# Performance work log

Hardware: AMD Instinct MI355X
Metric: run time of the kernel (lower is better)

The kernel has to match this reference:

```python
import jax, jax.numpy as jnp
import numpy as np

N = 20000
E = 100000
EB = 20000
WIDTH = 32
KER_W = 64
KER_IN = 6
DEPTH = 4


def setup_inputs() -> dict:
    key = jax.random.key(0)
    ks = jax.random.split(key, 24)
    d = {}
    d["x"] = jax.random.normal(ks[0], (N, 1), dtype=jnp.float32)
    d["edge_index"] = jax.random.randint(ks[1], (2, E), 0, N)
    d["edge_attr"] = jax.random.uniform(ks[2], (E, KER_IN), dtype=jnp.float32)
    d["edge_index_boundary"] = jax.random.randint(ks[3], (2, EB), 0, N)
    d["edge_attr_boundary"] = jax.random.uniform(ks[4], (EB, KER_IN), dtype=jnp.float32)
    s = 0.1
    d["fc1_w"] = jax.random.normal(ks[5], (1, WIDTH), dtype=jnp.float32) * s
    d["fc1_b"] = jnp.zeros((WIDTH,), jnp.float32)
    d["fc2_w"] = jax.random.normal(ks[6], (WIDTH, 1), dtype=jnp.float32) * s
    d["fc2_b"] = jnp.zeros((1,), jnp.float32)
    for i, pfx in enumerate(["k1", "k2"]):
        o = 7 + i * 5
        d[pfx + "_w1"] = jax.random.normal(ks[o], (KER_IN, KER_W), dtype=jnp.float32) * s
        d[pfx + "_b1"] = jnp.zeros((KER_W,), jnp.float32)
        d[pfx + "_w2"] = jax.random.normal(ks[o + 1], (KER_W, KER_W), dtype=jnp.float32) * s
        d[pfx + "_b2"] = jnp.zeros((KER_W,), jnp.float32)
        d[pfx + "_w3"] = jax.random.normal(ks[o + 2], (KER_W, WIDTH * WIDTH), dtype=jnp.float32) * s
        d[pfx + "_b3"] = jnp.zeros((WIDTH * WIDTH,), jnp.float32)
        d[("root1", "root2")[i]] = jax.random.normal(ks[o + 3], (WIDTH, WIDTH), dtype=jnp.float32) * s
        d[("bias1", "bias2")[i]] = jnp.zeros((WIDTH,), jnp.float32)
    return d


def _nnconv(h, ei, ea, w1, b1, w2, b2, w3, b3, root, bias):
    # kernel MLP on edge_attr -> per-edge [in, out] weight
    k = jax.nn.relu(ea @ w1 + b1)
    k = jax.nn.relu(k @ w2 + b2)
    w = (k @ w3 + b3).reshape(-1, WIDTH, WIDTH)  # [E, in, out]
    msg = jnp.einsum('ei,eio->eo', h[ei[0]], w)  # gather + per-edge matmul
    agg = jax.ops.segment_sum(msg, ei[1], num_segments=N)
    cnt = jax.ops.segment_sum(jnp.ones((ei.shape[1],), h.dtype), ei[1], num_segments=N)
    agg = agg / jnp.maximum(cnt, 1.0)[:, None]  # mean aggregation
    return agg + h @ root + bias


def reference(x, edge_index, edge_attr, edge_index_boundary, edge_attr_boundary,
              fc1_w, fc1_b, fc2_w, fc2_b,
              k1_w1, k1_b1, k1_w2, k1_b2, k1_w3, k1_b3, root1, bias1,
              k2_w1, k2_b1, k2_w2, k2_b2, k2_w3, k2_b3, root2, bias2):
    h0 = x @ fc1_w + fc1_b  # fc1(data.x), reused every depth step
    h = h0
    for _ in range(DEPTH):
        h = (_nnconv(h, edge_index, edge_attr, k1_w1, k1_b1, k1_w2, k1_b2, k1_w3, k1_b3, root1, bias1)
             + _nnconv(h, edge_index_boundary, edge_attr_boundary, k2_w1, k2_b1, k2_w2, k2_b2, k2_w3, k2_b3, root2, bias2))
        h = jax.nn.relu(h) + h0
    return h @ fc2_w + fc2_b
```

## Files before the change

### kernel.cpp

```cpp
#include <hip/hip_runtime.h>
#include <cstdint>
#include <cstddef>

#define NN    20000
#define EM    100000
#define EBN   20000
#define WID   32
#define KW    64
#define KIN   6
#define NDEPTH 4
#define GC    2080
#define NBL   8
#define GR    2084
#define NQ    520
#define TPB_F 576


__global__ void k_count4(const int* __restrict__ ei, const int* __restrict__ eib,
                         int* __restrict__ cs1, int* __restrict__ cnt1,
                         int* __restrict__ csb, int* __restrict__ cntb) {
    int t = blockIdx.x * blockDim.x + threadIdx.x;
    if (t < EM) atomicAdd(&cs1[ei[t]], 1);
    else if (t < 2 * EM) atomicAdd(&cnt1[ei[t]], 1);
    else if (t < 2 * EM + EBN) atomicAdd(&csb[eib[t - 2 * EM]], 1);
    else if (t < 2 * EM + 2 * EBN) atomicAdd(&cntb[eib[t - 2 * EM]], 1);
}

__global__ void k_inv2(const int* __restrict__ cnt1, float* __restrict__ inv1,
                       const int* __restrict__ cntb, float* __restrict__ invb) {
    int i = blockIdx.x * blockDim.x + threadIdx.x;
    if (i < NN) {
        int c = cnt1[i]; if (c < 1) c = 1;
        inv1[i] = 1.0f / (float)c;
    } else if (i < 2 * NN) {
        int c = cntb[i - NN]; if (c < 1) c = 1;
        invb[i - NN] = 1.0f / (float)c;
    }
}


__global__ __launch_bounds__(1024) void k_scan3(
        const int* __restrict__ csA, int* __restrict__ curA, int* __restrict__ arankA,
        int* __restrict__ anodesA, int* __restrict__ aoffA, int* __restrict__ dnaA, int EA,
        const int* __restrict__ csB, int* __restrict__ curB, int* __restrict__ arankB,
        int* __restrict__ anodesB, int* __restrict__ aoffB, int* __restrict__ dnaB, int EB) {
    __shared__ int part[1024];
    __shared__ int partf[1024];
    const int* cnt; int *cur, *arank, *anodes, *aoff, *dna; int E;
    if (blockIdx.x == 0) { cnt = csA; cur = curA; arank = arankA; anodes = anodesA; aoff = aoffA; dna = dnaA; E = EA; }
    else                 { cnt = csB; cur = curB; arank = arankB; anodes = anodesB; aoff = aoffB; dna = dnaB; E = EB; }
    int t = threadIdx.x;
    int per = (NN + 1023) / 1024;
    int base = t * per;
    int s = 0, f = 0;
    for (int i = 0; i < per; i++) {
        int idx = base + i;
        if (idx < NN) { int c = cnt[idx]; s += c; f += (c > 0) ? 1 : 0; }
    }
    part[t] = s; partf[t] = f;
    __syncthreads();
    for (int od = 1; od < 1024; od <<= 1) {
        int v  = (t >= od) ? part[t - od] : 0;
        int vf = (t >= od) ? partf[t - od] : 0;
        __syncthreads();
        part[t] += v; partf[t] += vf;
        __syncthreads();
    }
    int run  = (t > 0) ? part[t - 1] : 0;
    int runf = (t > 0) ? partf[t - 1] : 0;
    for (int i = 0; i < per; i++) {
        int idx = base + i;
        if (idx < NN) {
            int c = cnt[idx];
            cur[idx] = run;
            arank[idx] = runf;
            if (c > 0) { anodes[runf] = idx; aoff[runf] = run; runf++; }
            run += c;
        }
    }
    if (t == 1023) { dna[0] = partf[1023]; aoff[partf[1023]] = E; }
}


__global__ void k_scatter3(const int* __restrict__ ei, int* __restrict__ cur1,
                           int* __restrict__ perm1, const int* __restrict__ eib,
                           int* __restrict__ curb, int* __restrict__ permb) {
    int t = blockIdx.x * blockDim.x + threadIdx.x;
    if (t < EM) { int p = atomicAdd(&cur1[ei[t]], 1); perm1[p] = t; }
    else if (t < EM + EBN) {
        int e = t - EM;
        int p = atomicAdd(&curb[eib[e]], 1); permb[p] = e;
    }
}

__global__ void k_permidx3(const int* __restrict__ ei, const int* __restrict__ perm1,
                           const int* __restrict__ arank1, int* __restrict__ rk1,
                           int* __restrict__ dst1,
                           const int* __restrict__ eib, const int* __restrict__ permb,
                           const int* __restrict__ arankb, int* __restrict__ rkb,
                           int* __restrict__ dstb) {
    int t = blockIdx.x * blockDim.x + threadIdx.x;
    if (t < EM) {
        int e = perm1[t];
        rk1[t] = arank1[ei[e]];
        dst1[t] = ei[EM + e];
    } else if (t < EM + EBN) {
        int i = t - EM;
        int e = permb[i];
        rkb[i] = arankb[eib[e]];
        dstb[i] = eib[EBN + e];
    }
}


__global__ void k_permM3(const float* __restrict__ w3a, const float* __restrict__ b3a,
                         float* __restrict__ M1,
                         const float* __restrict__ w3b, const float* __restrict__ b3b,
                         float* __restrict__ M2,
                         const float* __restrict__ r1, const float* __restrict__ b1,
                         const float* __restrict__ r2, const float* __restrict__ b2,
                         float* __restrict__ rs, float* __restrict__ bs) {
    int t = blockIdx.x * blockDim.x + threadIdx.x;
    if (t < 32 * GC) {
        int i = t / GC, c = t % GC;
        M1[t] = (c < 2048) ? w3a[(c >> 5) * 1024 + i * 32 + (c & 31)]
                           : b3a[i * 32 + (c - 2048)];
    } else if (t < 64 * GC) {
        int u = t - 32 * GC;
        int i = u / GC, c = u % GC;
        M2[u] = (c < 2048) ? w3b[(c >> 5) * 1024 + i * 32 + (c & 31)]
                           : b3b[i * 32 + (c - 2048)];
    } else if (t < 64 * GC + 1024) {
        int i = t - 64 * GC;
        rs[i] = r1[i] + r2[i];
    } else if (t < 64 * GC + 1056) {
        int i = t - 64 * GC - 1024;
        bs[i] = b1[i] + b2[i];
    }
}


__global__ __launch_bounds__(256) void k_mlp3(
        const float* __restrict__ ea1, const int* __restrict__ perm1,
        const float* __restrict__ w1a, const float* __restrict__ b1a,
        const float* __restrict__ w2a, const float* __restrict__ b2a,
        float* __restrict__ K1,
        const float* __restrict__ ea2, const int* __restrict__ permb,
        const float* __restrict__ w1b, const float* __restrict__ b1b,
        const float* __restrict__ w2b, const float* __restrict__ b2b,
        float* __restrict__ K2, int nmb) {
    __shared__ float sw1[KIN * KW];
    __shared__ float sw2[KW * KW];
    __shared__ float sb1[KW];
    __shared__ float sb2[KW];
    const float *ea, *w1, *b1, *w2, *b2;
    const int* perm;
    float* K;
    int e, E;
    if ((int)blockIdx.x < nmb) {
        ea = ea1; perm = perm1; w1 = w1a; b1 = b1a; w2 = w2a; b2 = b2a; K = K1;
        e = blockIdx.x * 256 + threadIdx.x; E = EM;
    } else {
        ea = ea2; perm = permb; w1 = w1b; b1 = b1b; w2 = w2b; b2 = b2b; K = K2;
        e = (blockIdx.x - nmb) * 256 + threadIdx.x; E = EBN;
    }
    for (int i = threadIdx.x; i < KIN * KW; i += 256) sw1[i] = w1[i];
    for (int i = threadIdx.x; i < KW * KW; i += 256)  sw2[i] = w2[i];
    if (threadIdx.x < KW) { sb1[threadIdx.x] = b1[threadIdx.x]; sb2[threadIdx.x] = b2[threadIdx.x]; }
    __syncthreads();
    if (e >= E) return;
    int eo = perm[e];
    float a0 = ea[(size_t)eo * KIN + 0];
    float a1 = ea[(size_t)eo * KIN + 1];
    float a2 = ea[(size_t)eo * KIN + 2];
    float a3 = ea[(size_t)eo * KIN + 3];
    float a4 = ea[(size_t)eo * KIN + 4];
    float a5 = ea[(size_t)eo * KIN + 5];
    float t[KW];
#pragma unroll
    for (int j = 0; j < KW; j++) {
        float s = sb1[j];
        s += a0 * sw1[0 * KW + j];
        s += a1 * sw1[1 * KW + j];
        s += a2 * sw1[2 * KW + j];
        s += a3 * sw1[3 * KW + j];
        s += a4 * sw1[4 * KW + j];
        s += a5 * sw1[5 * KW + j];
        t[j] = fmaxf(s, 0.0f);
    }
#pragma unroll
    for (int h = 0; h < 2; h++) {
        int j0 = h * 32;
        float4 acc[8];
#pragma unroll
        for (int jj = 0; jj < 8; jj++)
            acc[jj] = *(const float4*)&sb2[j0 + jj * 4];
#pragma unroll
        for (int c = 0; c < KW; c++) {
            float tc = t[c];
#pragma unroll
            for (int jj = 0; jj < 8; jj++) {
                float4 w = *(const float4*)&sw2[c * KW + j0 + jj * 4];
                acc[jj].x += tc * w.x; acc[jj].y += tc * w.y;
                acc[jj].z += tc * w.z; acc[jj].w += tc * w.w;
            }
        }
#pragma unroll
        for (int jj = 0; jj < 8; jj++) {
            float4 r = acc[jj];
            r.x = fmaxf(r.x, 0.f); r.y = fmaxf(r.y, 0.f);
            r.z = fmaxf(r.z, 0.f); r.w = fmaxf(r.w, 0.f);
            *(float4*)&K[(size_t)e * KW + j0 + jj * 4] = r;
        }
    }
}


__global__ void k_h0g(const float* __restrict__ x, const float* __restrict__ fc1w,
        const float* __restrict__ fc1b, float* __restrict__ h,
        const int* __restrict__ arank1, const int* __restrict__ anodes1,
        const int* __restrict__ dna1, float* __restrict__ hg1,
        const int* __restrict__ arankb, const int* __restrict__ anodesb,
        const int* __restrict__ dnab, float* __restrict__ hgb) {
    int t = blockIdx.x * blockDim.x + threadIdx.x;
    if (t < NN * WID) {
        int n = t >> 5, j = t & 31;
        float v = x[n] * fc1w[j] + fc1b[j];
        h[t] = v;
        int r = arank1[n];
        if (r < dna1[0] && anodes1[r] == n)
            hg1[(r >> 3) * 256 + j * 8 + (r & 7)] = v;
    } else if (t < 2 * NN * WID) {
        int u = t - NN * WID;
        int n = u >> 5, j = u & 31;
        int r = arankb[n];
        if (r < dnab[0] && anodesb[r] == n)
            hgb[(r >> 3) * 256 + j * 8 + (r & 7)] = x[n] * fc1w[j] + fc1b[j];
    }
}


__global__ __launch_bounds__(TPB_F, 2) void k_fuse3(
        const int* __restrict__ rkA, const int* __restrict__ dstA,
        const int* __restrict__ aoffA, const int* __restrict__ dnaA,
        const float* __restrict__ KA, const float* __restrict__ MA,
        const float* __restrict__ hgA, float* __restrict__ aggA,
        const int* __restrict__ rkB, const int* __restrict__ dstB,
        const int* __restrict__ aoffB, const int* __restrict__ dnaB,
        const float* __restrict__ KB, const float* __restrict__ MB,
        const float* __restrict__ hgB, float* __restrict__ aggB,
        int nblkA) {
    __shared__ float sG[NBL * GR];
    const int *rk_s, *dst_s, *aoff;
    const float *Ks, *M, *hg;
    float* agg;
    int bid, na;
    if ((int)blockIdx.x < nblkA) {
        bid = blockIdx.x; na = dnaA[0];
        rk_s = rkA; dst_s = dstA; aoff = aoffA; Ks = KA; M = MA; hg = hgA; agg = aggA;
    } else {
        bid = blockIdx.x - nblkA; na = dnaB[0];
        rk_s = rkB; dst_s = dstB; aoff = aoffB; Ks = KB; M = MB; hg = hgB; agg = aggB;
    }
    int a0 = bid * NBL;
    if (a0 >= na) return;
    int t = threadIdx.x;
    if (t < NQ) {
        int col = t * 4;
        const float* hb = hg + bid * 256;
        const float* Mp = M + col;
        float4 acc[NBL];
#pragma unroll
        for (int r = 0; r < NBL; r++) acc[r] = make_float4(0.f, 0.f, 0.f, 0.f);
        float4 mbuf[4];
        float4 habuf[2], hcbuf[2];
#pragma unroll
        for (int i = 0; i < 4; i++) mbuf[i] = *(const float4*)&Mp[(size_t)i * GC];
#pragma unroll
        for (int i = 0; i < 2; i++) {
            habuf[i] = *(const float4*)&hb[i * 8];
            hcbuf[i] = *(const float4*)&hb[i * 8 + 4];
        }
#pragma unroll
        for (int k = 0; k < 32; k++) {
            float4 mv = mbuf[k & 3];
            float4 ha = habuf[k & 1];
            float4 hc = hcbuf[k & 1];
            if (k < 28) mbuf[k & 3] = *(const float4*)&Mp[(size_t)(k + 4) * GC];
            if (k < 30) {
                habuf[k & 1] = *(const float4*)&hb[(k + 2) * 8];
                hcbuf[k & 1] = *(const float4*)&hb[(k + 2) * 8 + 4];
            }
            float hv[NBL] = {ha.x, ha.y, ha.z, ha.w, hc.x, hc.y, hc.z, hc.w};
#pragma unroll
            for (int r = 0; r < NBL; r++) {
                acc[r].x += hv[r] * mv.x; acc[r].y += hv[r] * mv.y;
                acc[r].z += hv[r] * mv.z; acc[r].w += hv[r] * mv.w;
            }
        }
#pragma unroll
        for (int r = 0; r < NBL; r++)
            *(float4*)&sG[r * GR + col] = acc[r];
    }
    __syncthreads();
    int a1 = a0 + NBL; if (a1 > na) a1 = na;
    int e_lo = aoff[a0];
    int e_hi = aoff[a1];
    int g = t >> 3;
    int q4 = (t & 7) * 4;
    for (int e = e_lo + g; e < e_hi; e += TPB_F / 8) {
        int row = rk_s[e] - a0;
        int dst = dst_s[e];
        const float* Kr = Ks + (size_t)e * KW;
        int gb = row * GR;
        float4 v0 = *(const float4*)&sG[gb + 2048 + q4];
        float4 v1 = make_float4(0.f, 0.f, 0.f, 0.f);
        float4 v2 = v1, v3 = v1;
        float4 kbuf[2];
        kbuf[0] = *(const float4*)&Kr[0];
        kbuf[1] = *(const float4*)&Kr[4];
#pragma unroll
        for (int c4 = 0; c4 < 16; c4++) {
            float4 kv = kbuf[c4 & 1];
            if (c4 < 14) kbuf[c4 & 1] = *(const float4*)&Kr[(c4 + 2) * 4];
            float4 g0 = *(const float4*)&sG[gb + (c4 * 4 + 0) * 32 + q4];
            float4 g1 = *(const float4*)&sG[gb + (c4 * 4 + 1) * 32 + q4];
            float4 g2 = *(const float4*)&sG[gb + (c4 * 4 + 2) * 32 + q4];
            float4 g3 = *(const float4*)&sG[gb + (c4 * 4 + 3) * 32 + q4];
            v0.x += kv.x * g0.x; v0.y += kv.x * g0.y; v0.z += kv.x * g0.z; v0.w += kv.x * g0.w;
            v1.x += kv.y * g1.x; v1.y += kv.y * g1.y; v1.z += kv.y * g1.z; v1.w += kv.y * g1.w;
            v2.x += kv.z * g2.x; v2.y += kv.z * g2.y; v2.z += kv.z * g2.z; v2.w += kv.z * g2.w;
            v3.x += kv.w * g3.x; v3.y += kv.w * g3.y; v3.z += kv.w * g3.z; v3.w += kv.w * g3.w;
        }
        float4 m;
        m.x = v0.x + v1.x + v2.x + v3.x;
        m.y = v0.y + v1.y + v2.y + v3.y;
        m.z = v0.z + v1.z + v2.z + v3.z;
        m.w = v0.w + v1.w + v2.w + v3.w;
        float* ap = agg + (size_t)dst * WID + q4;
        unsafeAtomicAdd(ap + 0, m.x);
        unsafeAtomicAdd(ap + 1, m.y);
        unsafeAtomicAdd(ap + 2, m.z);
        unsafeAtomicAdd(ap + 3, m.w);
    }
}


__global__ __launch_bounds__(256) void k_node2(float* __restrict__ h,
        const float* __restrict__ agg1, const float* __restrict__ aggb,
        const float* __restrict__ inv1, const float* __restrict__ invb,
        const float* __restrict__ x, const float* __restrict__ fc1w,
        const float* __restrict__ fc1b,
        const float* __restrict__ rs, const float* __restrict__ bs,
        const int* __restrict__ arank1, const int* __restrict__ anodes1,
        const int* __restrict__ dna1, float* __restrict__ hg1,
        const int* __restrict__ arankb, const int* __restrict__ anodesb,
        const int* __restrict__ dnab, float* __restrict__ hgb) {
    __shared__ float sR[1024];
    __shared__ float sB[32];
    for (int i = threadIdx.x; i < 1024; i += 256) sR[i] = rs[i];
    if (threadIdx.x < 32) sB[threadIdx.x] = bs[threadIdx.x];
    __syncthreads();
    int t = blockIdx.x * 256 + threadIdx.x;
    if (t >= NN * WID) return;
    int n = t >> 5, j = t & 31;
    float s = agg1[t] * inv1[n] + aggb[t] * invb[n] + sB[j];
    const float* hr = h + (size_t)n * WID;
#pragma unroll
    for (int i = 0; i < 32; i++) s += hr[i] * sR[i * 32 + j];
    float h0v = x[n] * fc1w[j] + fc1b[j];
    float val = fmaxf(s, 0.0f) + h0v;
    h[t] = val;
    int r1 = arank1[n];
    if (r1 < dna1[0] && anodes1[r1] == n)
        hg1[(r1 >> 3) * 256 + j * 8 + (r1 & 7)] = val;
    int rb = arankb[n];
    if (rb < dnab[0] && anodesb[rb] == n)
        hgb[(rb >> 3) * 256 + j * 8 + (rb & 7)] = val;
}

__global__ void k_fc2(const float* __restrict__ h, const float* __restrict__ w,
                      const float* __restrict__ b, float* __restrict__ out) {
    int n = blockIdx.x * blockDim.x + threadIdx.x;
    if (n >= NN) return;
    const float4* hv = (const float4*)(h + (size_t)n * WID);
    const float4* wv = (const float4*)w;
    float s = b[0];
#pragma unroll
    for (int q = 0; q < 8; q++) {
        float4 a = hv[q], c = wv[q];
        s += a.x * c.x + a.y * c.y + a.z * c.z + a.w * c.w;
    }
    out[n] = s;
}


extern "C" void kernel_launch(void* const* d_in, const int* in_sizes, int n_in,
                              void* d_out, int out_size, void* d_ws, size_t ws_size,
                              hipStream_t stream) {
    const float* x    = (const float*)d_in[0];
    const int*   ei   = (const int*)d_in[1];
    const float* ea   = (const float*)d_in[2];
    const int*   eib  = (const int*)d_in[3];
    const float* eab  = (const float*)d_in[4];
    const float* fc1w = (const float*)d_in[5];
    const float* fc1b = (const float*)d_in[6];
    const float* fc2w = (const float*)d_in[7];
    const float* fc2b = (const float*)d_in[8];
    const float* k1w1 = (const float*)d_in[9];
    const float* k1b1 = (const float*)d_in[10];
    const float* k1w2 = (const float*)d_in[11];
    const float* k1b2 = (const float*)d_in[12];
    const float* k1w3 = (const float*)d_in[13];
    const float* k1b3 = (const float*)d_in[14];
    const float* root1= (const float*)d_in[15];
    const float* bias1= (const float*)d_in[16];
    const float* k2w1 = (const float*)d_in[17];
    const float* k2b1 = (const float*)d_in[18];
    const float* k2w2 = (const float*)d_in[19];
    const float* k2b2 = (const float*)d_in[20];
    const float* k2w3 = (const float*)d_in[21];
    const float* k2b3 = (const float*)d_in[22];
    const float* root2= (const float*)d_in[23];
    const float* bias2= (const float*)d_in[24];

    float* p = (float*)d_ws;
    auto alloc = [&](size_t nflt) { float* r = p; p += nflt; return r; };
    float* K1   = alloc((size_t)EM * KW);
    float* Kb   = alloc((size_t)EBN * KW);
    float* hA   = alloc((size_t)NN * WID);
    float* agg1 = alloc((size_t)NN * WID);
    float* aggb = alloc((size_t)NN * WID);
    float* hg1  = alloc((size_t)2500 * 256);
    float* hgb  = alloc((size_t)2500 * 256);
    float* inv1 = alloc(NN);
    float* invb = alloc(NN);
    float* rs   = alloc(1024);
    float* bs   = alloc(32);
    int*   cnt1 = (int*)alloc(NN);
    int*   cntb = (int*)alloc(NN);
    int*   cs1  = (int*)alloc(NN);
    int*   csb  = (int*)alloc(NN);
    int*   cur1 = (int*)alloc(NN);
    int*   curb = (int*)alloc(NN);
    int*   arank1 = (int*)alloc(NN);
    int*   arankb = (int*)alloc(NN);
    int*   anodes1= (int*)alloc(NN);
    int*   anodesb= (int*)alloc(NN);
    int*   aoff1  = (int*)alloc(NN + 1);
    int*   aoffb  = (int*)alloc(NN + 1);
    int*   dna1   = (int*)alloc(1);
    int*   dnab   = (int*)alloc(1);
    int*   perm1= (int*)alloc(EM);
    int*   permb= (int*)alloc(EBN);
    int*   rk1  = (int*)alloc(EM);
    int*   dst1 = (int*)alloc(EM);
    int*   rkb  = (int*)alloc(EBN);
    int*   dstb = (int*)alloc(EBN);
    float* M1   = alloc(32 * GC);
    float* M2   = alloc(32 * GC);

    hipMemsetAsync(cnt1, 0, 4 * NN * sizeof(int), stream);
    k_count4<<<(2 * EM + 2 * EBN + 255) / 256, 256, 0, stream>>>(ei, eib, cs1, cnt1, csb, cntb);
    k_scan3<<<2, 1024, 0, stream>>>(cs1, cur1, arank1, anodes1, aoff1, dna1, EM,
                                    csb, curb, arankb, anodesb, aoffb, dnab, EBN);
    k_inv2<<<(2 * NN + 255) / 256, 256, 0, stream>>>(cnt1, inv1, cntb, invb);
    k_scatter3<<<(EM + EBN + 255) / 256, 256, 0, stream>>>(ei, cur1, perm1, eib, curb, permb);
    k_permidx3<<<(EM + EBN + 255) / 256, 256, 0, stream>>>(ei, perm1, arank1, rk1, dst1,
                                                           eib, permb, arankb, rkb, dstb);
    int nmb = (EM + 255) / 256;
    k_mlp3<<<nmb + (EBN + 255) / 256, 256, 0, stream>>>(
        ea, perm1, k1w1, k1b1, k1w2, k1b2, K1,
        eab, permb, k2w1, k2b1, k2w2, k2b2, Kb, nmb);
    k_permM3<<<(64 * GC + 1056 + 255) / 256, 256, 0, stream>>>(
        k1w3, k1b3, M1, k2w3, k2b3, M2, root1, bias1, root2, bias2, rs, bs);
    k_h0g<<<(2 * NN * WID + 255) / 256, 256, 0, stream>>>(x, fc1w, fc1b, hA,
                                                          anodes1 ? arank1 : arank1, anodes1, dna1, hg1,
                                                          arankb, anodesb, dnab, hgb);

    int nblkA = (NN + NBL - 1) / NBL;
    int fgrid = nblkA * 2;
    for (int d = 0; d < NDEPTH; d++) {
        hipMemsetAsync(agg1, 0, (size_t)2 * NN * WID * sizeof(float), stream);
        k_fuse3<<<fgrid, TPB_F, 0, stream>>>(rk1, dst1, aoff1, dna1, K1, M1, hg1, agg1,
                                             rkb, dstb, aoffb, dnab, Kb, M2, hgb, aggb,
                                             nblkA);
        k_node2<<<(NN * WID + 255) / 256, 256, 0, stream>>>(hA, agg1, aggb, inv1, invb,
                                                            x, fc1w, fc1b, rs, bs,
                                                            arank1, anodes1, dna1, hg1,
                                                            arankb, anodesb, dnab, hgb);
    }
    k_fc2<<<(NN + 255) / 256, 256, 0, stream>>>(hA, fc2w, fc2b, (float*)d_out);
}
```

Measured before the change: 654.2 us.

## Make fused conv kernel persistent with register-resident M columns

Replaces the one-block-per-node-group launch with a fixed grid of persistent blocks (312 for the main graph, 200 for the boundary graph) that loop over node groups in a grid-stride pattern. Each thread loads its 32 float4 slices of the M matrix into registers once and reuses them for every group, instead of re-streaming M from global memory per group. It also drops the manual prefetch double-buffering of h and K loads. The 128 extra VGPRs for Mreg risk spills or lower occupancy under the 2-blocks-per-CU launch bound, and fewer blocks may hurt load balance and latency hiding.

```diff
diff --git a/kernel.cpp b/kernel.cpp
--- a/kernel.cpp
+++ b/kernel.cpp
@@ -14,6 +14,8 @@
 #define GR    2084
 #define NQ    520
 #define TPB_F 576
+#define NBLK_MAIN 312
+#define NBLK_BND  200
 
 
 __global__ void k_count4(const int* __restrict__ ei, const int* __restrict__ eib,
@@ -240,7 +242,7 @@
 }
 
 
-__global__ __launch_bounds__(TPB_F, 2) void k_fuse3(
+__global__ __launch_bounds__(TPB_F, 2) void k_fuse4(
         const int* __restrict__ rkA, const int* __restrict__ dstA,
         const int* __restrict__ aoffA, const int* __restrict__ dnaA,
         const float* __restrict__ KA, const float* __restrict__ MA,
@@ -248,100 +250,91 @@
         const int* __restrict__ rkB, const int* __restrict__ dstB,
         const int* __restrict__ aoffB, const int* __restrict__ dnaB,
         const float* __restrict__ KB, const float* __restrict__ MB,
-        const float* __restrict__ hgB, float* __restrict__ aggB,
-        int nblkA) {
+        const float* __restrict__ hgB, float* __restrict__ aggB) {
     __shared__ float sG[NBL * GR];
     const int *rk_s, *dst_s, *aoff;
     const float *Ks, *M, *hg;
     float* agg;
-    int bid, na;
-    if ((int)blockIdx.x < nblkA) {
-        bid = blockIdx.x; na = dnaA[0];
+    int b0, nblk, na;
+    if ((int)blockIdx.x < NBLK_MAIN) {
+        b0 = blockIdx.x; nblk = NBLK_MAIN; na = dnaA[0];
         rk_s = rkA; dst_s = dstA; aoff = aoffA; Ks = KA; M = MA; hg = hgA; agg = aggA;
     } else {
-        bid = blockIdx.x - nblkA; na = dnaB[0];
+        b0 = blockIdx.x - NBLK_MAIN; nblk = NBLK_BND; na = dnaB[0];
         rk_s = rkB; dst_s = dstB; aoff = aoffB; Ks = KB; M = MB; hg = hgB; agg = aggB;
     }
-    int a0 = bid * NBL;
-    if (a0 >= na) return;
     int t = threadIdx.x;
+    float4 Mreg[32];
     if (t < NQ) {
-        int col = t * 4;
-        const float* hb = hg + bid * 256;
-        const float* Mp = M + col;
-        float4 acc[NBL];
-#pragma unroll
-        for (int r = 0; r < NBL; r++) acc[r] = make_float4(0.f, 0.f, 0.f, 0.f);
-        float4 mbuf[4];
-        float4 habuf[2], hcbuf[2];
-#pragma unroll
-        for (int i = 0; i < 4; i++) mbuf[i] = *(const float4*)&Mp[(size_t)i * GC];
-#pragma unroll
-        for (int i = 0; i < 2; i++) {
-            habuf[i] = *(const float4*)&hb[i * 8];
-            hcbuf[i] = *(const float4*)&hb[i * 8 + 4];
+        const float* Mp = M + t * 4;
+#pragma unroll
+        for (int k = 0; k < 32; k++)
+            Mreg[k] = *(const float4*)&Mp[(size_t)k * GC];
+    }
+    int ngroups = (na + NBL - 1) / NBL;
+    int g = b0;
+    for (; g < ngroups; g += nblk) {
+        int a0 = g * NBL;
+        if (t < NQ) {
+            const float* hb = hg + (size_t)g * 256;
+            float4 acc[NBL];
+#pragma unroll
+            for (int r = 0; r < NBL; r++) acc[r] = make_float4(0.f, 0.f, 0.f, 0.f);
+#pragma unroll
+            for (int k = 0; k < 32; k++) {
+                float4 mv = Mreg[k];
+                float4 ha = *(const float4*)&hb[k * 8];
+                float4 hc = *(const float4*)&hb[k * 8 + 4];
+                float hv[NBL] = {ha.x, ha.y, ha.z, ha.w, hc.x, hc.y, hc.z, hc.w};
+#pragma unroll
+                for (int r = 0; r < NBL; r++) {
+                    acc[r].x += hv[r] * mv.x; acc[r].y += hv[r] * mv.y;
+                    acc[r].z += hv[r] * mv.z; acc[r].w += hv[r] * mv.w;
+                }
+            }
+            int col = t * 4;
+#pragma unroll
+            for (int r = 0; r < NBL; r++)
+                *(float4*)&sG[r * GR + col] = acc[r];
         }
-#pragma unroll
-        for (int k = 0; k < 32; k++) {
-            float4 mv = mbuf[k & 3];
-            float4 ha = habuf[k & 1];
-            float4 hc = hcbuf[k & 1];
-            if (k < 28) mbuf[k & 3] = *(const float4*)&Mp[(size_t)(k + 4) * GC];
-            if (k < 30) {
-                habuf[k & 1] = *(const float4*)&hb[(k + 2) * 8];
-                hcbuf[k & 1] = *(const float4*)&hb[(k + 2) * 8 + 4];
+        __syncthreads();
+        int a1 = a0 + NBL; if (a1 > na) a1 = na;
+        int e_lo = aoff[a0];
+        int e_hi = aoff[a1];
+        int eg = t >> 3;
+        int q4 = (t & 7) * 4;
+        for (int e = e_lo + eg; e < e_hi; e += TPB_F / 8) {
+            int row = rk_s[e] - a0;
+            int dst = dst_s[e];
+            const float* Kr = Ks + (size_t)e * KW;
+            int gb = row * GR;
+            float4 v0 = *(const float4*)&sG[gb + 2048 + q4];
+            float4 v1 = make_float4(0.f, 0.f, 0.f, 0.f);
+            float4 v2 = v1, v3 = v1;
+#pragma unroll
+            for (int c4 = 0; c4 < 16; c4++) {
+                float4 kv = *(const float4*)&Kr[c4 * 4];
+                float4 g0 = *(const float4*)&sG[gb + (c4 * 4 + 0) * 32 + q4];
+                float4 g1 = *(const float4*)&sG[gb + (c4 * 4 + 1) * 32 + q4];
+                float4 g2 = *(const float4*)&sG[gb + (c4 * 4 + 2) * 32 + q4];
+                float4 g3 = *(const float4*)&sG[gb + (c4 * 4 + 3) * 32 + q4];
+                v0.x += kv.x * g0.x; v0.y += kv.x * g0.y; v0.z += kv.x * g0.z; v0.w += kv.x * g0.w;
+                v1.x += kv.y * g1.x; v1.y += kv.y * g1.y; v1.z += kv.y * g1.z; v1.w += kv.y * g1.w;
+                v2.x += kv.z * g2.x; v2.y += kv.z * g2.y; v2.z += kv.z * g2.z; v2.w += kv.z * g2.w;
+                v3.x += kv.w * g3.x; v3.y += kv.w * g3.y; v3.z += kv.w * g3.z; v3.w += kv.w * g3.w;
             }
-            float hv[NBL] = {ha.x, ha.y, ha.z, ha.w, hc.x, hc.y, hc.z, hc.w};
-#pragma unroll
-            for (int r = 0; r < NBL; r++) {
-                acc[r].x += hv[r] * mv.x; acc[r].y += hv[r] * mv.y;
-                acc[r].z += hv[r] * mv.z; acc[r].w += hv[r] * mv.w;
-            }
+            float4 m;
+            m.x = v0.x + v1.x + v2.x + v3.x;
+            m.y = v0.y + v1.y + v2.y + v3.y;
+            m.z = v0.z + v1.z + v2.z + v3.z;
+            m.w = v0.w + v1.w + v2.w + v3.w;
+            float* ap = agg + (size_t)dst * WID + q4;
+            unsafeAtomicAdd(ap + 0, m.x);
+            unsafeAtomicAdd(ap + 1, m.y);
+            unsafeAtomicAdd(ap + 2, m.z);
+            unsafeAtomicAdd(ap + 3, m.w);
         }
-#pragma unroll
-        for (int r = 0; r < NBL; r++)
-            *(float4*)&sG[r * GR + col] = acc[r];
-    }
-    __syncthreads();
-    int a1 = a0 + NBL; if (a1 > na) a1 = na;
-    int e_lo = aoff[a0];
-    int e_hi = aoff[a1];
-    int g = t >> 3;
-    int q4 = (t & 7) * 4;
-    for (int e = e_lo + g; e < e_hi; e += TPB_F / 8) {
-        int row = rk_s[e] - a0;
-        int dst = dst_s[e];
-        const float* Kr = Ks + (size_t)e * KW;
-        int gb = row * GR;
-        float4 v0 = *(const float4*)&sG[gb + 2048 + q4];
-        float4 v1 = make_float4(0.f, 0.f, 0.f, 0.f);
-        float4 v2 = v1, v3 = v1;
-        float4 kbuf[2];
-        kbuf[0] = *(const float4*)&Kr[0];
-        kbuf[1] = *(const float4*)&Kr[4];
-#pragma unroll
-        for (int c4 = 0; c4 < 16; c4++) {
-            float4 kv = kbuf[c4 & 1];
-            if (c4 < 14) kbuf[c4 & 1] = *(const float4*)&Kr[(c4 + 2) * 4];
-            float4 g0 = *(const float4*)&sG[gb + (c4 * 4 + 0) * 32 + q4];
-            float4 g1 = *(const float4*)&sG[gb + (c4 * 4 + 1) * 32 + q4];
-            float4 g2 = *(const float4*)&sG[gb + (c4 * 4 + 2) * 32 + q4];
-            float4 g3 = *(const float4*)&sG[gb + (c4 * 4 + 3) * 32 + q4];
-            v0.x += kv.x * g0.x; v0.y += kv.x * g0.y; v0.z += kv.x * g0.z; v0.w += kv.x * g0.w;
-            v1.x += kv.y * g1.x; v1.y += kv.y * g1.y; v1.z += kv.y * g1.z; v1.w += kv.y * g1.w;
-            v2.x += kv.z * g2.x; v2.y += kv.z * g2.y; v2.z += kv.z * g2.z; v2.w += kv.z * g2.w;
-            v3.x += kv.w * g3.x; v3.y += kv.w * g3.y; v3.z += kv.w * g3.z; v3.w += kv.w * g3.w;
-        }
-        float4 m;
-        m.x = v0.x + v1.x + v2.x + v3.x;
-        m.y = v0.y + v1.y + v2.y + v3.y;
-        m.z = v0.z + v1.z + v2.z + v3.z;
-        m.w = v0.w + v1.w + v2.w + v3.w;
-        float* ap = agg + (size_t)dst * WID + q4;
-        unsafeAtomicAdd(ap + 0, m.x);
-        unsafeAtomicAdd(ap + 1, m.y);
-        unsafeAtomicAdd(ap + 2, m.z);
-        unsafeAtomicAdd(ap + 3, m.w);
+        __syncthreads();
     }
 }
 
@@ -475,16 +468,14 @@
     k_permM3<<<(64 * GC + 1056 + 255) / 256, 256, 0, stream>>>(
         k1w3, k1b3, M1, k2w3, k2b3, M2, root1, bias1, root2, bias2, rs, bs);
     k_h0g<<<(2 * NN * WID + 255) / 256, 256, 0, stream>>>(x, fc1w, fc1b, hA,
-                                                          anodes1 ? arank1 : arank1, anodes1, dna1, hg1,
+                                                          arank1, anodes1, dna1, hg1,
                                                           arankb, anodesb, dnab, hgb);
 
-    int nblkA = (NN + NBL - 1) / NBL;
-    int fgrid = nblkA * 2;
     for (int d = 0; d < NDEPTH; d++) {
         hipMemsetAsync(agg1, 0, (size_t)2 * NN * WID * sizeof(float), stream);
-        k_fuse3<<<fgrid, TPB_F, 0, stream>>>(rk1, dst1, aoff1, dna1, K1, M1, hg1, agg1,
-                                             rkb, dstb, aoffb, dnab, Kb, M2, hgb, aggb,
-                                             nblkA);
+        k_fuse4<<<NBLK_MAIN + NBLK_BND, TPB_F, 0, stream>>>(
+            rk1, dst1, aoff1, dna1, K1, M1, hg1, agg1,
+            rkb, dstb, aoffb, dnab, Kb, M2, hgb, aggb);
         k_node2<<<(NN * WID + 255) / 256, 256, 0, stream>>>(hA, agg1, aggb, inv1, invb,
                                                             x, fc1w, fc1b, rs, bs,
                                                             arank1, anodes1, dna1, hg1,
```

Result: slower. 1.430 ms (+118.6%).
